# Kernel optimization log

Measured on AMD Instinct MI355X. Metric: run time of the kernel, lower is better.

## Reference

```python
import jax, jax.numpy as jnp
import numpy as np

NG = 64  # number of graphs in the batch (global_add_pool output rows)

def _bn(x, g, b):
    # BatchNorm1d, training-mode batch statistics over dim 0
    mu = x.mean(0)
    var = x.var(0)
    return (x - mu) * jax.lax.rsqrt(var + 1e-5) * g + b

def _ln(x, g, b):
    mu = x.mean(-1, keepdims=True)
    var = x.var(-1, keepdims=True)
    return (x - mu) * jax.lax.rsqrt(var + 1e-5) * g + b

def _gine(x, ei, ea, eps, w1, b1, w2, b2, n):
    # GINEConv: mlp((1+eps)*x + sum_dst ReLU(x[src] + ea))
    msg = jax.nn.relu(x[ei[0]] + ea)
    agg = jax.ops.segment_sum(msg, ei[1], num_segments=n)
    h = (1.0 + eps) * x + agg
    return jax.nn.relu(h @ w1 + b1) @ w2 + b2

def setup_inputs() -> dict:
    key = jax.random.key(0)
    H, L, RW = 128, 4, 16
    Nn, m, kk = 4096, 2, 32
    S = Nn * m; SK = S * kk
    Ei, Eg = 1048576, 65536
    Vatom, Vbond = 128, 16
    ks = jax.random.split(key, 24)
    f = lambda i, shape: jax.random.normal(ks[i], shape, jnp.float32) * 0.02
    # intra edges sampled within each subgraph block to honor locality
    subs = jax.random.randint(ks[11], (Ei,), 0, S)
    src = subs * kk + jax.random.randint(ks[12], (Ei,), 0, kk)
    dst = subs * kk + jax.random.randint(ks[13], (Ei,), 0, kk)
    inp = {
        "atom_emb": f(0, (Vatom, H)), "bond_emb": f(1, (Vbond, H)),
        "rwse_w": f(2, (RW, H)), "rwse_b": jnp.zeros((H,), jnp.float32),
        "rwse": jax.random.uniform(ks[3], (Nn, RW), jnp.float32),
        "l_eps": jnp.zeros((L,), jnp.float32),
        "l_w1": f(4, (L, H, H)), "l_b1": jnp.zeros((L, H), jnp.float32),
        "l_w2": f(5, (L, H, H)), "l_b2": jnp.zeros((L, H), jnp.float32),
        "l_bng": jnp.ones((L, H), jnp.float32), "l_bnb": jnp.zeros((L, H), jnp.float32),
        "g_eps": jnp.zeros((L,), jnp.float32),
        "g_w1": f(6, (L, H, H)), "g_b1": jnp.zeros((L, H), jnp.float32),
        "g_w2": f(7, (L, H, H)), "g_b2": jnp.zeros((L, H), jnp.float32),
        "g_bng": jnp.ones((L, H), jnp.float32), "g_bnb": jnp.zeros((L, H), jnp.float32),
        "bcast_w": f(8, (L, H, H)),
        "cat_w1": f(9, (L, 2 * H, H)), "cat_b1": jnp.zeros((L, H), jnp.float32),
        "cat_w2": f(10, (L, H, H)), "cat_b2": jnp.zeros((L, H), jnp.float32),
        "ln_g": jnp.ones((L, H), jnp.float32), "ln_b": jnp.zeros((L, H), jnp.float32),
        "x_ids": jax.random.randint(ks[14], (SK,), 0, Vatom),
        "intra_ei": jnp.stack([src, dst]),
        "intra_ea_ids": jax.random.randint(ks[15], (Ei,), 0, Vbond),
        "global_ei": jax.random.randint(ks[16], (2, Eg), 0, Nn),
        "global_ea_ids": jax.random.randint(ks[17], (Eg,), 0, Vbond),
        "node_ids": jax.random.randint(ks[18], (SK,), 0, Nn),
        "valid": jax.random.randint(ks[19], (SK,), 0, 2),
        "batch": jnp.sort(jax.random.randint(ks[20], (Nn,), 0, NG)),
        "k": 32,
    }
    return inp

def reference(atom_emb, bond_emb, rwse_w, rwse_b, rwse, l_eps, l_w1, l_b1, l_w2, l_b2, l_bng, l_bnb, g_eps, g_w1, g_b1, g_w2, g_b2, g_bng, g_bnb, bcast_w, cat_w1, cat_b1, cat_w2, cat_b2, ln_g, ln_b, x_ids, intra_ei, intra_ea_ids, global_ei, global_ea_ids, node_ids, valid, batch, k):
    SK = x_ids.shape[0]; Nn = rwse.shape[0]
    S = SK // k; m = S // Nn
    H = atom_emb.shape[1]; L = l_eps.shape[0]
    ea_flat = bond_emb[intra_ea_ids]          # [Ei, H]
    g_ea = bond_emb[global_ea_ids]            # [Eg, H]
    valid_f = valid.astype(jnp.float32)[:, None]
    h = (atom_emb[x_ids] + jax.nn.relu(rwse @ rwse_w + rwse_b)[node_ids]) * valid_f  # [SK, H]
    node_assign = jnp.repeat(jnp.arange(Nn), m)   # [S]
    root_idx = jnp.arange(S) * k                  # subgraph roots in flat layout
    for i in range(L):
        h_in = h
        h_local = _bn(jax.nn.relu(_gine(h, intra_ei, ea_flat, l_eps[i], l_w1[i], l_b1[i], l_w2[i], l_b2[i], SK)), l_bng[i], l_bnb[i])
        # scatter-mean of root reps onto original nodes (each node has exactly m subgraphs)
        h_node = jax.ops.segment_sum(h[root_idx], node_assign, num_segments=Nn) / m
        h_cross = _bn(jax.nn.relu(_gine(h_node, global_ei, g_ea, g_eps[i], g_w1[i], g_b1[i], g_w2[i], g_b2[i], Nn)), g_bng[i], g_bnb[i])
        h_node = h_node + h_cross
        # broadcast projected node reps back to every flat subgraph position
        h_b = jnp.repeat((h_node @ bcast_w[i])[node_assign], k, axis=0)  # [SK, H]
        h_cat = jnp.concatenate([h_local, h_b], axis=-1)
        h_new = _ln(jax.nn.gelu(h_cat @ cat_w1[i] + cat_b1[i], approximate=False) @ cat_w2[i] + cat_b2[i], ln_g[i], ln_b[i])
        h = (h_in + h_new) * valid_f
    # per-subgraph masked mean (h is already zero at invalid rows)
    cnt = valid_f.reshape(S, k, 1).sum(1)
    h_sub = h.reshape(S, k, H).sum(1) / jnp.maximum(cnt, 1.0)   # [S, H]
    h_nodef = h_sub.reshape(Nn, m, H).mean(1)                   # [Nn, H]
    return jax.ops.segment_sum(h_nodef, batch, num_segments=NG) # [NG, H]
```

## Files before the change

### kernel.cpp

```cpp
#include <hip/hip_runtime.h>
#include <hip/hip_bf16.h>

#define H 128
#define HH 16384
#define LNUM 4
#define NN 4096
#define SS 8192
#define SKK 262144
#define EI 1048576
#define EG 65536
#define NGRAPH 64

typedef unsigned short u16;
typedef unsigned int u32;
typedef __attribute__((ext_vector_type(8))) short s16x8;
typedef __attribute__((ext_vector_type(4))) float f32x4;

__device__ __forceinline__ float b2f(u32 u){ return __uint_as_float(u<<16); }
__device__ __forceinline__ u16 f2b(float f){
  union { __hip_bfloat16 b; u16 u; } x;
  x.b=__float2bfloat16(f);
  return x.u;
}
__device__ __forceinline__ void unp8(uint4 v, float* f){
  f[0]=b2f(v.x&0xFFFF); f[1]=b2f(v.x>>16);
  f[2]=b2f(v.y&0xFFFF); f[3]=b2f(v.y>>16);
  f[4]=b2f(v.z&0xFFFF); f[5]=b2f(v.z>>16);
  f[6]=b2f(v.w&0xFFFF); f[7]=b2f(v.w>>16);
}
__device__ __forceinline__ void unp4(uint2 v, float* f){
  f[0]=b2f(v.x&0xFFFF); f[1]=b2f(v.x>>16);
  f[2]=b2f(v.y&0xFFFF); f[3]=b2f(v.y>>16);
}
__device__ __forceinline__ uint4 pk8(const float* f){
  uint4 r;
  r.x=(u32)f2b(f[0])|((u32)f2b(f[1])<<16);
  r.y=(u32)f2b(f[2])|((u32)f2b(f[3])<<16);
  r.z=(u32)f2b(f[4])|((u32)f2b(f[5])<<16);
  r.w=(u32)f2b(f[6])|((u32)f2b(f[7])<<16);
  return r;
}
__device__ __forceinline__ uint2 pk4(const float* f){
  uint2 r;
  r.x=(u32)f2b(f[0])|((u32)f2b(f[1])<<16);
  r.y=(u32)f2b(f[2])|((u32)f2b(f[3])<<16);
  return r;
}

struct CvtArgs {
  const void* p[26];
  int start[27];
};
struct TransArgs { int src[28]; };

__global__ void k_sniff(const u16* __restrict__ a, int* __restrict__ flag){
  __shared__ int cnt;
  if(threadIdx.x==0) cnt=0;
  __syncthreads();
  int big=0;
  for(int i=threadIdx.x;i<2048;i+=256){
    int e=(a[i]>>7)&0xFF;
    if(e>=127) big++;
  }
  atomicAdd(&cnt,big);
  __syncthreads();
  if(threadIdx.x==0) *flag=(cnt<16)?1:0;
}

__global__ void k_convert(CvtArgs args, const int* __restrict__ flag, float* __restrict__ dst){
  int fl=*flag;
  int total=args.start[26];
  for(int i=blockIdx.x*blockDim.x+threadIdx.x;i<total;i+=gridDim.x*blockDim.x){
    int a=0;
    while(args.start[a+1]<=i) a++;
    int j=i-args.start[a];
    float v;
    if(fl) v=b2f(((const u16*)args.p[a])[j]);
    else   v=((const float*)args.p[a])[j];
    dst[i]=v;
  }
}

__global__ __launch_bounds__(256) void k_trans(const float* __restrict__ par, TransArgs ta, u16* __restrict__ wt){
  const float* s=par+ta.src[blockIdx.x];
  u16* d=wt+(size_t)blockIdx.x*HH;
  for(int i=threadIdx.x;i<HH;i+=256){
    int j=i&7, lane=(i>>3)&63, fc=i>>9;
    int n=fc>>2, kc=fc&3, lr=lane&15, lk=lane>>4;
    int outc=n*16+lr, k=kc*32+lk*8+j;
    d[i]=f2b(s[(size_t)k*H+outc]);
  }
}

__global__ void k_cvtbond(const float* __restrict__ b, u16* __restrict__ bb){
  int i=blockIdx.x*blockDim.x+threadIdx.x;
  if(i<16*H) bb[i]=f2b(b[i]);
}

__global__ __launch_bounds__(128) void k_prepw3(const float* __restrict__ w, const float* __restrict__ cb1,
                        const float* __restrict__ stl, const float* __restrict__ gl, const float* __restrict__ bl,
                        u16* __restrict__ wt3p, float* __restrict__ bias3){
  __shared__ float red[128];
  int c=blockIdx.x, k=threadIdx.x;
  float mu=stl[k]*(1.f/262144.f);
  float var=stl[128+k]*(1.f/262144.f)-mu*mu;
  float s=gl[k]*rsqrtf(var+1e-5f);
  float tt=bl[k]-mu*s;
  float wv=w[(size_t)k*H+c];
  int idx=(((c>>4)*4+(k>>5))*64+((k>>3)&3)*16+(c&15))*8+(k&7);
  wt3p[idx]=f2b(s*wv);
  red[k]=tt*wv;
  __syncthreads();
  for(int d=64;d>0;d>>=1){ if(k<d) red[k]+=red[k+d]; __syncthreads(); }
  if(k==0) bias3[c]=cb1[c]+red[0];
}

__global__ void k_hist(const int* __restrict__ idx, int n, int shift, int* __restrict__ cnt){
  for(int i=blockIdx.x*blockDim.x+threadIdx.x;i<n;i+=gridDim.x*blockDim.x)
    atomicAdd(&cnt[idx[i]>>shift],1);
}

__global__ void k_scan(const int* __restrict__ cnt, int* __restrict__ off, int nbins){
  __shared__ int ts[1024];
  int t=threadIdx.x;
  int per=nbins>>10;
  int base=t*per;
  int s=0;
  for(int j=0;j<per;j++) s+=cnt[base+j];
  ts[t]=s;
  __syncthreads();
  for(int d=1;d<1024;d<<=1){
    int v=(t>=d)?ts[t-d]:0;
    __syncthreads();
    ts[t]+=v;
    __syncthreads();
  }
  int ex=(t==0)?0:ts[t-1];
  for(int j=0;j<per;j++){ off[base+j]=ex; ex+=cnt[base+j]; }
}

__global__ void k_scatter_i(const int* __restrict__ ei, const int* __restrict__ ea,
                            const int* __restrict__ off, int* __restrict__ cur, int* __restrict__ pack){
  for(int i=blockIdx.x*blockDim.x+threadIdx.x;i<EI;i+=gridDim.x*blockDim.x){
    int s=ei[i], d=ei[EI+i];
    int sub=d>>5;
    int pos=off[sub]+atomicAdd(&cur[sub],1);
    pack[pos]=((s&31)<<9)|((d&31)<<4)|(ea[i]&15);
  }
}

__global__ __launch_bounds__(128) void k_sortsub(const int* __restrict__ eoff, const int* __restrict__ ecnt,
                                                 int* __restrict__ epack, int* __restrict__ dstoff){
  __shared__ int ein[512];
  __shared__ int eout[512];
  __shared__ int bcnt[32];
  __shared__ int bpos[32];
  int sub=blockIdx.x, t=threadIdx.x;
  int o=eoff[sub];
  int n=ecnt[sub]; if(n>512) n=512;
  for(int i=t;i<n;i+=128) ein[i]=epack[o+i];
  if(t<32) bcnt[t]=0;
  __syncthreads();
  for(int i=t;i<n;i+=128) atomicAdd(&bcnt[(ein[i]>>4)&31],1);
  __syncthreads();
  if(t==0){
    int s=0;
    for(int b=0;b<32;b++){ bpos[b]=s; s+=bcnt[b]; }
  }
  __syncthreads();
  if(t<32) dstoff[sub*32+t]=bpos[t];
  __syncthreads();
  for(int i=t;i<n;i+=128){
    int p=ein[i];
    int pos=atomicAdd(&bpos[(p>>4)&31],1);
    eout[pos]=p;
  }
  __syncthreads();
  for(int i=t;i<n;i+=128) epack[o+i]=eout[i];
}

__global__ void k_scatter_g(const int* __restrict__ ei, const int* __restrict__ ea,
                            const int* __restrict__ off, int* __restrict__ cur, int* __restrict__ pack){
  for(int i=blockIdx.x*blockDim.x+threadIdx.x;i<EG;i+=gridDim.x*blockDim.x){
    int s=ei[i], d=ei[EG+i];
    int pos=off[d]+atomicAdd(&cur[d],1);
    pack[pos]=(s<<4)|(ea[i]&15);
  }
}

__global__ __launch_bounds__(128) void k_rwse(const float* __restrict__ rwse, const float* __restrict__ w,
                      const float* __restrict__ b, float* __restrict__ rf){
  __shared__ float ws[16*128];
  __shared__ float rv[16];
  int n=blockIdx.x, c=threadIdx.x;
  for(int i=c;i<2048;i+=128) ws[i]=w[i];
  if(c<16) rv[c]=rwse[n*16+c];
  __syncthreads();
  float acc=b[c];
  for(int j=0;j<16;j++) acc=fmaf(rv[j],ws[j*128+c],acc);
  rf[(size_t)n*H+c]=fmaxf(acc,0.f);
}

template<int MODE>
__global__ __launch_bounds__(256,4) void k_fused1(
    const u16* __restrict__ h, const u16* __restrict__ beb,
    const int* __restrict__ eoff, const int* __restrict__ ecnt, const int* __restrict__ epack,
    const int* __restrict__ dstoff,
    const float* __restrict__ epsp, int layer,
    const u16* __restrict__ W1p, const float* __restrict__ b1,
    const u16* __restrict__ W2p, const float* __restrict__ b2,
    u16* __restrict__ Xg, float* __restrict__ stats,
    const u16* __restrict__ W3p, const float* __restrict__ bias3,
    const u16* __restrict__ bbv,
    const u16* __restrict__ Wc2p, const float* __restrict__ cb2,
    const float* __restrict__ lng, const float* __restrict__ lnb,
    const int* __restrict__ validv, u16* __restrict__ hio,
    const float* __restrict__ atomp, const float* __restrict__ rfp,
    const int* __restrict__ xids, const int* __restrict__ nids,
    u16* __restrict__ hnOut)
{
  __shared__ u16 hs[64*128];
  __shared__ u16 agx[64*128];
  __shared__ u16 bes[16*128];
  __shared__ u16 epku[2][512];
  __shared__ int doff[2][32];
  float* sst=(float*)&epku[0][0];

  int t=threadIdx.x;
  int grp=t>>7, c=t&127;
  size_t hbase=(size_t)blockIdx.x*64*H;
  int wave=t>>6, lane=t&63, lr=lane&15, lk=lane>>4;
  int rl=wave*16+lr;
  u32 rsw=((u32)(rl&7))<<4;
  int row0=blockIdx.x*64;

  {
    u32 row=(u32)(t>>4), colb=(u32)((t&15)*16);
    *(uint4*)((char*)bes+row*256+(colb^((row&7)<<4)))=((const uint4*)beb)[t];
  }
  int sub=blockIdx.x*2+grp;
  int n=min(ecnt[sub],512);
  int o=eoff[sub];
  if(c<32) doff[grp][c]=dstoff[sub*32+c];
  for(int i=c;i<n;i+=128) epku[grp][i]=(u16)epack[o+i];

  if(MODE==1){
    f32x4 a1t[8];
    #pragma unroll
    for(int n8=0;n8<8;n8++) a1t[n8]=(f32x4){0.f,0.f,0.f,0.f};
    const s16x8* B0=(const s16x8*)(Xg+(size_t)(row0+rl)*H);
    #pragma unroll
    for(int kc=0;kc<4;kc++){
      s16x8 bf=B0[kc*4+lk];
      #pragma unroll
      for(int n8=0;n8<8;n8++){
        s16x8 af=*(const s16x8*)(W3p+((n8*4+kc)<<9)+lane*8);
        a1t[n8]=__builtin_amdgcn_mfma_f32_16x16x32_bf16(af,bf,a1t[n8],0,0,0);
      }
    }
    #pragma unroll
    for(int n8=0;n8<8;n8++){
      int c0=n8*16+lk*4;
      float4 b4=*(const float4*)(bias3+c0);
      float rb[4];
      unp4(*(const uint2*)(bbv+(size_t)blockIdx.x*H+c0),rb);
      float vb[4]={b4.x,b4.y,b4.z,b4.w};
      float v[4];
      #pragma unroll
      for(int j=0;j<4;j++){
        float x=a1t[n8][j]+vb[j]+rb[j];
        v[j]=0.5f*x*(1.f+erff(x*0.70710678118654752f));
      }
      *(uint2*)((char*)agx+(u32)rl*256+(((u32)(2*c0))^rsw))=pk4(v);
    }
    f32x4 a2t[8];
    #pragma unroll
    for(int n8=0;n8<8;n8++) a2t[n8]=(f32x4){0.f,0.f,0.f,0.f};
    #pragma unroll
    for(int kc=0;kc<4;kc++){
      u32 cb=(u32)((kc*32+lk*8)*2);
      s16x8 bf=*(const s16x8*)((char*)agx+(u32)rl*256+(cb^rsw));
      #pragma unroll
      for(int n8=0;n8<8;n8++){
        s16x8 af=*(const s16x8*)(Wc2p+((n8*4+kc)<<9)+lane*8);
        a2t[n8]=__builtin_amdgcn_mfma_f32_16x16x32_bf16(af,bf,a2t[n8],0,0,0);
      }
    }
    {
      float s=0.f,q=0.f;
      #pragma unroll
      for(int n8=0;n8<8;n8++){
        int c0=n8*16+lk*4;
        float4 b4=*(const float4*)(cb2+c0);
        float vb[4]={b4.x,b4.y,b4.z,b4.w};
        #pragma unroll
        for(int j=0;j<4;j++){
          float v=a2t[n8][j]+vb[j];
          a2t[n8][j]=v;
          s+=v; q+=v*v;
        }
      }
      s+=__shfl_xor(s,16); s+=__shfl_xor(s,32);
      q+=__shfl_xor(q,16); q+=__shfl_xor(q,32);
      float mu=s*(1.f/128.f);
      float rsig=rsqrtf(q*(1.f/128.f)-mu*mu+1e-5f);
      #pragma unroll
      for(int n8=0;n8<8;n8++){
        int c0=n8*16+lk*4;
        float4 g4=*(const float4*)(lng+c0);
        float4 e4=*(const float4*)(lnb+c0);
        float g[4]={g4.x,g4.y,g4.z,g4.w}, e[4]={e4.x,e4.y,e4.z,e4.w};
        float ov[4];
        #pragma unroll
        for(int j=0;j<4;j++) ov[j]=(a2t[n8][j]-mu)*rsig*g[j]+e[j];
        *(uint2*)((char*)agx+(u32)rl*256+(((u32)(2*c0))^rsw))=pk4(ov);
      }
    }
    __syncthreads();
    uint4* hp=(uint4*)(hio+hbase);
    #pragma unroll
    for(int p=0;p<4;p++){
      int i=t+p*256;
      u32 row=(u32)(i>>4), colb=(u32)((i&15)*16);
      int grow=row0+(int)row;
      uint4 v=*(const uint4*)((const char*)agx+row*256+(colb^((row&7)<<4)));
      uint4 r=hp[i];
      float vv[8],rv[8],o8[8];
      unp8(v,vv); unp8(r,rv);
      float vm=validv[grow]?1.f:0.f;
      #pragma unroll
      for(int j=0;j<8;j++) o8[j]=(rv[j]+vv[j])*vm;
      uint4 pk=pk8(o8);
      hp[i]=pk;
      *(uint4*)((char*)hs+row*256+(colb^((row&7)<<4)))=pk;
    }
  } else {
    int r=t>>2, q=t&3;
    int grow=row0+r;
    float vm=validv[grow]?1.f:0.f;
    const float4* ap=(const float4*)(atomp+(size_t)xids[grow]*H)+q*8;
    const float4* bp=(const float4*)(rfp+(size_t)nids[grow]*H)+q*8;
    u32 rowsw=((u32)(r&7))<<4;
    uint4* hgp=(uint4*)(hio+hbase);
    #pragma unroll
    for(int k=0;k<4;k++){
      float4 a0=ap[k*2], a1=ap[k*2+1], b0=bp[k*2], b1=bp[k*2+1];
      float f[8]={(a0.x+b0.x)*vm,(a0.y+b0.y)*vm,(a0.z+b0.z)*vm,(a0.w+b0.w)*vm,
                  (a1.x+b1.x)*vm,(a1.y+b1.y)*vm,(a1.z+b1.z)*vm,(a1.w+b1.w)*vm};
      uint4 pk=pk8(f);
      u32 cb=(u32)(q*64+k*16);
      *(uint4*)((char*)hs+(u32)r*256+(cb^rowsw))=pk;
      hgp[r*16+q*4+k]=pk;
    }
  }
  __syncthreads();

  if(t<16){
    uint4 aR=*(const uint4*)((const char*)hs+(u32)t*16);
    uint4 bR=*(const uint4*)((const char*)hs+32*256+(u32)t*16);
    float fa[8],fb[8],fo[8];
    unp8(aR,fa); unp8(bR,fb);
    #pragma unroll
    for(int j=0;j<8;j++) fo[j]=0.5f*(fa[j]+fb[j]);
    ((uint4*)(hnOut+(size_t)blockIdx.x*H))[t]=pk8(fo);
  }
  {
    float ep=1.f+epsp[layer];
    #pragma unroll
    for(int p=0;p<4;p++){
      int i=t+p*256;
      u32 row=(u32)(i>>4), colb=(u32)((i&15)*16);
      u32 off=row*256+(colb^((row&7)<<4));
      float hf[8],o8[8];
      unp8(*(const uint4*)((const char*)hs+off),hf);
      #pragma unroll
      for(int j=0;j<8;j++) o8[j]=ep*hf[j];
      *(uint4*)((char*)agx+off)=pk8(o8);
    }
  }
  __syncthreads();

  {
    int slot=c>>4, chg=c&15;
    u32 cbyte=(u32)chg*16;
    int d0=slot*4;
    int s0=doff[grp][d0];
    int send=(d0+3==31)?n:doff[grp][d0+4];
    const u16* ep_=&epku[grp][0];
    auto LDP=[&](int p, uint4& hv, uint4& bv){
      u32 srow=(u32)(grp*32+(p>>9));
      u32 erow=(u32)(p&15);
      hv=*(const uint4*)((const char*)hs+srow*256+(cbyte^((srow&7)<<4)));
      bv=*(const uint4*)((const char*)bes+erow*256+(cbyte^((erow&7)<<4)));
    };
    auto FLUSH=[&](int cur, float* acc){
      u32 drow=(u32)(grp*32+cur);
      u32 aoff=drow*256+(cbyte^((drow&7)<<4));
      float of[8];
      unp8(*(const uint4*)((const char*)agx+aoff),of);
      #pragma unroll
      for(int q=0;q<8;q++) of[q]+=acc[q];
      *(uint4*)((char*)agx+aoff)=pk8(of);
    };
    float acc[8]={0.f,0.f,0.f,0.f,0.f,0.f,0.f,0.f};
    int cur=-1;
    uint4 hvA,bvA,hvB,bvB;
    hvA=bvA=hvB=bvB=make_uint4(0,0,0,0);
    int pA=0,pB=0;
    if(s0<send){ pA=ep_[s0]; LDP(pA,hvA,bvA); }
    if(s0+1<send){ pB=ep_[s0+1]; LDP(pB,hvB,bvB); }
    for(int j=s0;j<send;){
      {
        float hf[8],bf8[8];
        unp8(hvA,hf); unp8(bvA,bf8);
        int pc=pA;
        if(j+2<send){ pA=ep_[j+2]; LDP(pA,hvA,bvA); }
        int dl=(pc>>4)&31;
        if(dl!=cur){
          if(cur>=0) FLUSH(cur,acc);
          #pragma unroll
          for(int q=0;q<8;q++) acc[q]=0.f;
          cur=dl;
        }
        #pragma unroll
        for(int q=0;q<8;q++) acc[q]+=fmaxf(hf[q]+bf8[q],0.f);
      }
      j++;
      if(j>=send) break;
      {
        float hf[8],bf8[8];
        unp8(hvB,hf); unp8(bvB,bf8);
        int pc=pB;
        if(j+2<send){ pB=ep_[j+2]; LDP(pB,hvB,bvB); }
        int dl=(pc>>4)&31;
        if(dl!=cur){
          if(cur>=0) FLUSH(cur,acc);
          #pragma unroll
          for(int q=0;q<8;q++) acc[q]=0.f;
          cur=dl;
        }
        #pragma unroll
        for(int q=0;q<8;q++) acc[q]+=fmaxf(hf[q]+bf8[q],0.f);
      }
      j++;
    }
    if(cur>=0) FLUSH(cur,acc);
  }
  __syncthreads();
  sst[t]=0.f;
  __syncthreads();

  f32x4 a1[8];
  #pragma unroll
  for(int n8=0;n8<8;n8++) a1[n8]=(f32x4){0.f,0.f,0.f,0.f};
  #pragma unroll
  for(int kc=0;kc<4;kc++){
    u32 cb=(u32)((kc*32+lk*8)*2);
    s16x8 bf=*(const s16x8*)((char*)agx+(u32)rl*256+(cb^rsw));
    #pragma unroll
    for(int n8=0;n8<8;n8++){
      s16x8 af=*(const s16x8*)(W1p+((n8*4+kc)<<9)+lane*8);
      a1[n8]=__builtin_amdgcn_mfma_f32_16x16x32_bf16(af,bf,a1[n8],0,0,0);
    }
  }
  #pragma unroll
  for(int n8=0;n8<8;n8++){
    int c0=n8*16+lk*4;
    float4 b4=*(const float4*)(b1+c0);
    float v[4]={fmaxf(a1[n8][0]+b4.x,0.f),fmaxf(a1[n8][1]+b4.y,0.f),
                fmaxf(a1[n8][2]+b4.z,0.f),fmaxf(a1[n8][3]+b4.w,0.f)};
    *(uint2*)((char*)hs+(u32)rl*256+(((u32)(2*c0))^rsw))=pk4(v);
  }
  f32x4 a2[8];
  #pragma unroll
  for(int n8=0;n8<8;n8++) a2[n8]=(f32x4){0.f,0.f,0.f,0.f};
  #pragma unroll
  for(int kc=0;kc<4;kc++){
    u32 cb=(u32)((kc*32+lk*8)*2);
    s16x8 bf=*(const s16x8*)((char*)hs+(u32)rl*256+(cb^rsw));
    #pragma unroll
    for(int n8=0;n8<8;n8++){
      s16x8 af=*(const s16x8*)(W2p+((n8*4+kc)<<9)+lane*8);
      a2[n8]=__builtin_amdgcn_mfma_f32_16x16x32_bf16(af,bf,a2[n8],0,0,0);
    }
  }
  #pragma unroll
  for(int n8=0;n8<8;n8++){
    int c0=n8*16+lk*4;
    float4 b4=*(const float4*)(b2+c0);
    float v[4]={fmaxf(a2[n8][0]+b4.x,0.f),fmaxf(a2[n8][1]+b4.y,0.f),
                fmaxf(a2[n8][2]+b4.z,0.f),fmaxf(a2[n8][3]+b4.w,0.f)};
    *(uint2*)((char*)agx+(u32)rl*256+(((u32)(2*c0))^rsw))=pk4(v);
    float s[4],q[4];
    #pragma unroll
    for(int j2=0;j2<4;j2++){ s[j2]=v[j2]; q[j2]=v[j2]*v[j2]; }
    #pragma unroll
    for(int j2=0;j2<4;j2++){
      #pragma unroll
      for(int d=1;d<16;d<<=1){
        s[j2]+=__shfl_xor(s[j2],d);
        q[j2]+=__shfl_xor(q[j2],d);
      }
    }
    if(lr==0){
      #pragma unroll
      for(int j2=0;j2<4;j2++){
        atomicAdd(&sst[c0+j2],s[j2]);
        atomicAdd(&sst[128+c0+j2],q[j2]);
      }
    }
  }
  __syncthreads();
  uint4* out4=(uint4*)(Xg+hbase);
  #pragma unroll
  for(int p=0;p<4;p++){
    int i=t+p*256;
    u32 row=(u32)(i>>4), colb=(u32)((i&15)*16);
    out4[i]=*(const uint4*)((const char*)agx+row*256+(colb^((row&7)<<4)));
  }
  atomicAdd(&stats[t],sst[t]);
}

__global__ __launch_bounds__(256) void k_mlp2n(
    const u16* __restrict__ A, const u16* __restrict__ W1p, const float* __restrict__ b1,
    const u16* __restrict__ W2p, const float* __restrict__ b2,
    u16* __restrict__ out, float* __restrict__ stats)
{
  __shared__ u16 T[64*128];
  __shared__ float sst[256];
  int t=threadIdx.x;
  sst[t]=0.f;
  int wave=t>>6, lane=t&63, lr=lane&15, lk=lane>>4;
  int rl=wave*16+lr;
  u32 rsw=((u32)(rl&7))<<4;
  int row0=blockIdx.x*64;
  f32x4 a1[8];
  #pragma unroll
  for(int n8=0;n8<8;n8++) a1[n8]=(f32x4){0.f,0.f,0.f,0.f};
  const s16x8* B0=(const s16x8*)(A+(size_t)(row0+rl)*H);
  #pragma unroll
  for(int kc=0;kc<4;kc++){
    s16x8 bf=B0[kc*4+lk];
    #pragma unroll
    for(int n8=0;n8<8;n8++){
      s16x8 af=*(const s16x8*)(W1p+((n8*4+kc)<<9)+lane*8);
      a1[n8]=__builtin_amdgcn_mfma_f32_16x16x32_bf16(af,bf,a1[n8],0,0,0);
    }
  }
  #pragma unroll
  for(int n8=0;n8<8;n8++){
    int c0=n8*16+lk*4;
    float4 b4=*(const float4*)(b1+c0);
    float v[4]={fmaxf(a1[n8][0]+b4.x,0.f),fmaxf(a1[n8][1]+b4.y,0.f),
                fmaxf(a1[n8][2]+b4.z,0.f),fmaxf(a1[n8][3]+b4.w,0.f)};
    *(uint2*)((char*)T+(u32)rl*256+(((u32)(2*c0))^rsw))=pk4(v);
  }
  f32x4 a2[8];
  #pragma unroll
  for(int n8=0;n8<8;n8++) a2[n8]=(f32x4){0.f,0.f,0.f,0.f};
  #pragma unroll
  for(int kc=0;kc<4;kc++){
    u32 cb=(u32)((kc*32+lk*8)*2);
    s16x8 bf=*(const s16x8*)((char*)T+(u32)rl*256+(cb^rsw));
    #pragma unroll
    for(int n8=0;n8<8;n8++){
      s16x8 af=*(const s16x8*)(W2p+((n8*4+kc)<<9)+lane*8);
      a2[n8]=__builtin_amdgcn_mfma_f32_16x16x32_bf16(af,bf,a2[n8],0,0,0);
    }
  }
  #pragma unroll
  for(int n8=0;n8<8;n8++){
    int c0=n8*16+lk*4;
    float4 b4=*(const float4*)(b2+c0);
    float v[4]={fmaxf(a2[n8][0]+b4.x,0.f),fmaxf(a2[n8][1]+b4.y,0.f),
                fmaxf(a2[n8][2]+b4.z,0.f),fmaxf(a2[n8][3]+b4.w,0.f)};
    *(uint2*)((char*)T+(u32)rl*256+(((u32)(2*c0))^rsw))=pk4(v);
    float s[4],q[4];
    #pragma unroll
    for(int j=0;j<4;j++){ s[j]=v[j]; q[j]=v[j]*v[j]; }
    #pragma unroll
    for(int j=0;j<4;j++){
      #pragma unroll
      for(int d=1;d<16;d<<=1){
        s[j]+=__shfl_xor(s[j],d);
        q[j]+=__shfl_xor(q[j],d);
      }
    }
    if(lr==0){
      #pragma unroll
      for(int j=0;j<4;j++){
        atomicAdd(&sst[c0+j],s[j]);
        atomicAdd(&sst[128+c0+j],q[j]);
      }
    }
  }
  __syncthreads();
  uint4* out4=(uint4*)(out+(size_t)row0*H);
  #pragma unroll
  for(int p=0;p<4;p++){
    int i=t+p*256;
    u32 row=(u32)(i>>4), colb=(u32)((i&15)*16);
    out4[i]=*(const uint4*)((const char*)T+row*256+(colb^((row&7)<<4)));
  }
  atomicAdd(&stats[t],sst[t]);
}

__global__ __launch_bounds__(256) void k_bcast(
    const u16* __restrict__ hn, const u16* __restrict__ ag,
    const float* __restrict__ stg, const float* __restrict__ gg, const float* __restrict__ bg,
    const u16* __restrict__ Wbcp, const u16* __restrict__ Wc1p,
    u16* __restrict__ bb)
{
  __shared__ u16 T[64*128];
  __shared__ u16 T2[64*128];
  __shared__ float ssh[128], tsh[128];
  int t=threadIdx.x;
  int row0=blockIdx.x*64;
  if(t<128){
    float mu=stg[t]*(1.f/4096.f);
    float var=stg[128+t]*(1.f/4096.f)-mu*mu;
    float s=gg[t]*rsqrtf(var+1e-5f);
    ssh[t]=s; tsh[t]=bg[t]-mu*s;
  }
  __syncthreads();
  #pragma unroll
  for(int i0=0;i0<4;i0++){
    int i=t+i0*256;
    u32 row=(u32)(i>>4);
    int cb8=(i&15)*8;
    float hv[8],av[8],o8[8];
    unp8(((const uint4*)(hn+(size_t)row0*H))[i],hv);
    unp8(((const uint4*)(ag+(size_t)row0*H))[i],av);
    #pragma unroll
    for(int j=0;j<8;j++) o8[j]=hv[j]+fmaf(av[j],ssh[cb8+j],tsh[cb8+j]);
    *(uint4*)((char*)T+row*256+(((u32)(cb8*2))^((row&7)<<4)))=pk8(o8);
  }
  __syncthreads();
  int wave=t>>6, lane=t&63, lr=lane&15, lk=lane>>4;
  int rl=wave*16+lr;
  u32 rsw=((u32)(rl&7))<<4;
  f32x4 a1[8];
  #pragma unroll
  for(int n8=0;n8<8;n8++) a1[n8]=(f32x4){0.f,0.f,0.f,0.f};
  #pragma unroll
  for(int kc=0;kc<4;kc++){
    u32 cb=(u32)((kc*32+lk*8)*2);
    s16x8 bf=*(const s16x8*)((char*)T+(u32)rl*256+(cb^rsw));
    #pragma unroll
    for(int n8=0;n8<8;n8++){
      s16x8 af=*(const s16x8*)(Wbcp+((n8*4+kc)<<9)+lane*8);
      a1[n8]=__builtin_amdgcn_mfma_f32_16x16x32_bf16(af,bf,a1[n8],0,0,0);
    }
  }
  #pragma unroll
  for(int n8=0;n8<8;n8++){
    int c0=n8*16+lk*4;
    float v[4]={a1[n8][0],a1[n8][1],a1[n8][2],a1[n8][3]};
    *(uint2*)((char*)T2+(u32)rl*256+(((u32)(2*c0))^rsw))=pk4(v);
  }
  f32x4 a2[8];
  #pragma unroll
  for(int n8=0;n8<8;n8++) a2[n8]=(f32x4){0.f,0.f,0.f,0.f};
  #pragma unroll
  for(int kc=0;kc<4;kc++){
    u32 cb=(u32)((kc*32+lk*8)*2);
    s16x8 bf=*(const s16x8*)((char*)T2+(u32)rl*256+(cb^rsw));
    #pragma unroll
    for(int n8=0;n8<8;n8++){
      s16x8 af=*(const s16x8*)(Wc1p+((n8*4+kc)<<9)+lane*8);
      a2[n8]=__builtin_amdgcn_mfma_f32_16x16x32_bf16(af,bf,a2[n8],0,0,0);
    }
  }
  #pragma unroll
  for(int n8=0;n8<8;n8++){
    int c0=n8*16+lk*4;
    float v[4]={a2[n8][0],a2[n8][1],a2[n8][2],a2[n8][3]};
    *(uint2*)((char*)T+(u32)rl*256+(((u32)(2*c0))^rsw))=pk4(v);
  }
  __syncthreads();
  uint4* out4=(uint4*)(bb+(size_t)row0*H);
  #pragma unroll
  for(int p=0;p<4;p++){
    int i=t+p*256;
    u32 row=(u32)(i>>4), colb=(u32)((i&15)*16);
    out4[i]=*(const uint4*)((const char*)T+row*256+(colb^((row&7)<<4)));
  }
}

__global__ __launch_bounds__(128) void k_gagg(const u16* __restrict__ hn, const float* __restrict__ be,
                      const int* __restrict__ goff, const int* __restrict__ gcnt,
                      const int* __restrict__ gpack, const float* __restrict__ epsp, int layer,
                      u16* __restrict__ hhg){
  __shared__ float bes[16][128];
  int n=blockIdx.x, c=threadIdx.x;
  for(int i=0;i<16;i++) bes[i][c]=be[i*128+c];
  __syncthreads();
  float acc=0.f;
  int o=goff[n], e=o+gcnt[n];
  for(;o<e;o++){
    int p=gpack[o];
    acc+=fmaxf(b2f(hn[(size_t)(p>>4)*H+c])+bes[p&15][c],0.f);
  }
  hhg[(size_t)n*H+c]=f2b(fmaf(1.f+epsp[layer],b2f(hn[(size_t)n*H+c]),acc));
}

__global__ __launch_bounds__(256) void k_tailpool(
    const u16* __restrict__ X, const u16* __restrict__ W3p, const float* __restrict__ bias3,
    const u16* __restrict__ bb,
    const u16* __restrict__ W2p, const float* __restrict__ cb2,
    const float* __restrict__ lng, const float* __restrict__ lnb,
    const int* __restrict__ validv, const u16* __restrict__ hres,
    const int* __restrict__ batch, float* __restrict__ oacc)
{
  __shared__ u16 T[64*128];
  __shared__ float pbuf[256];
  __shared__ float cntsh[2];
  int t=threadIdx.x;
  int wave=t>>6, lane=t&63, lr=lane&15, lk=lane>>4;
  int rl=wave*16+lr;
  u32 rsw=((u32)(rl&7))<<4;
  int row0=blockIdx.x*64;
  f32x4 acc[8];
  #pragma unroll
  for(int n8=0;n8<8;n8++) acc[n8]=(f32x4){0.f,0.f,0.f,0.f};
  const s16x8* B0=(const s16x8*)(X+(size_t)(row0+rl)*H);
  #pragma unroll
  for(int kc=0;kc<4;kc++){
    s16x8 bf=B0[kc*4+lk];
    #pragma unroll
    for(int n8=0;n8<8;n8++){
      s16x8 af=*(const s16x8*)(W3p+((n8*4+kc)<<9)+lane*8);
      acc[n8]=__builtin_amdgcn_mfma_f32_16x16x32_bf16(af,bf,acc[n8],0,0,0);
    }
  }
  #pragma unroll
  for(int n8=0;n8<8;n8++){
    int c0=n8*16+lk*4;
    float4 b4=*(const float4*)(bias3+c0);
    float rb[4];
    unp4(*(const uint2*)(bb+(size_t)blockIdx.x*H+c0),rb);
    float vb[4]={b4.x,b4.y,b4.z,b4.w};
    float v[4];
    #pragma unroll
    for(int j=0;j<4;j++){
      float x=acc[n8][j]+vb[j]+rb[j];
      v[j]=0.5f*x*(1.f+erff(x*0.70710678118654752f));
    }
    *(uint2*)((char*)T+(u32)rl*256+(((u32)(2*c0))^rsw))=pk4(v);
  }
  f32x4 a2[8];
  #pragma unroll
  for(int n8=0;n8<8;n8++) a2[n8]=(f32x4){0.f,0.f,0.f,0.f};
  #pragma unroll
  for(int kc=0;kc<4;kc++){
    u32 cb=(u32)((kc*32+lk*8)*2);
    s16x8 bf=*(const s16x8*)((char*)T+(u32)rl*256+(cb^rsw));
    #pragma unroll
    for(int n8=0;n8<8;n8++){
      s16x8 af=*(const s16x8*)(W2p+((n8*4+kc)<<9)+lane*8);
      a2[n8]=__builtin_amdgcn_mfma_f32_16x16x32_bf16(af,bf,a2[n8],0,0,0);
    }
  }
  {
    float s=0.f,q=0.f;
    #pragma unroll
    for(int n8=0;n8<8;n8++){
      int c0=n8*16+lk*4;
      float4 b4=*(const float4*)(cb2+c0);
      float vb[4]={b4.x,b4.y,b4.z,b4.w};
      #pragma unroll
      for(int j=0;j<4;j++){
        float v=a2[n8][j]+vb[j];
        a2[n8][j]=v;
        s+=v; q+=v*v;
      }
    }
    s+=__shfl_xor(s,16); s+=__shfl_xor(s,32);
    q+=__shfl_xor(q,16); q+=__shfl_xor(q,32);
    float mu=s*(1.f/128.f);
    float rsig=rsqrtf(q*(1.f/128.f)-mu*mu+1e-5f);
    #pragma unroll
    for(int n8=0;n8<8;n8++){
      int c0=n8*16+lk*4;
      float4 g4=*(const float4*)(lng+c0);
      float4 e4=*(const float4*)(lnb+c0);
      float g[4]={g4.x,g4.y,g4.z,g4.w}, e[4]={e4.x,e4.y,e4.z,e4.w};
      float ov[4];
      #pragma unroll
      for(int j=0;j<4;j++) ov[j]=(a2[n8][j]-mu)*rsig*g[j]+e[j];
      *(uint2*)((char*)T+(u32)rl*256+(((u32)(2*c0))^rsw))=pk4(ov);
    }
  }
  pbuf[t]=0.f;
  if(t<2){
    int s=0;
    for(int j2=0;j2<32;j2++) s+=validv[row0+t*32+j2]?1:0;
    cntsh[t]=fmaxf((float)s,1.f);
  }
  __syncthreads();
  const uint4* hp=(const uint4*)(hres+(size_t)row0*H);
  float s0[8]={0,0,0,0,0,0,0,0}, s1[8]={0,0,0,0,0,0,0,0};
  #pragma unroll
  for(int p=0;p<4;p++){
    int i=t+p*256;
    u32 row=(u32)(i>>4), colb=(u32)((i&15)*16);
    int grow=row0+(int)row;
    uint4 v=*(const uint4*)((const char*)T+row*256+(colb^((row&7)<<4)));
    uint4 r=hp[i];
    float vv[8],rv[8];
    unp8(v,vv); unp8(r,rv);
    float vm=validv[grow]?1.f:0.f;
    #pragma unroll
    for(int j2=0;j2<8;j2++){
      float hn=(rv[j2]+vv[j2])*vm;
      if(p<2) s0[j2]+=hn; else s1[j2]+=hn;
    }
  }
  #pragma unroll
  for(int j2=0;j2<8;j2++){
    s0[j2]+=__shfl_xor(s0[j2],16); s0[j2]+=__shfl_xor(s0[j2],32);
    s1[j2]+=__shfl_xor(s1[j2],16); s1[j2]+=__shfl_xor(s1[j2],32);
  }
  if((lane&48)==0){
    int ch=(lane&15)*8;
    #pragma unroll
    for(int j2=0;j2<8;j2++){
      atomicAdd(&pbuf[ch+j2],s0[j2]);
      atomicAdd(&pbuf[128+ch+j2],s1[j2]);
    }
  }
  __syncthreads();
  if(t<128){
    float nodef=0.5f*(pbuf[t]/cntsh[0]+pbuf[128+t]/cntsh[1]);
    atomicAdd(&oacc[batch[blockIdx.x]*H+t],nodef);
  }
}

__global__ void k_out(const float* __restrict__ acc, const int* __restrict__ flag, void* __restrict__ out){
  int i=blockIdx.x*blockDim.x+threadIdx.x;
  if(i>=NGRAPH*H) return;
  if(*flag) ((__hip_bfloat16*)out)[i]=__float2bfloat16(acc[i]);
  else ((float*)out)[i]=acc[i];
}

extern "C" void kernel_launch(void* const* d_in, const int* in_sizes, int n_in,
                              void* d_out, int out_size, void* d_ws, size_t ws_size,
                              hipStream_t stream){
  (void)n_in; (void)out_size;
  int pofs[27]; pofs[0]=0;
  for(int i=0;i<26;i++) pofs[i+1]=pofs[i]+in_sizes[i];
  int ptot=pofs[26];

  char* wsb=(char*)d_ws;
  size_t off=0;
  auto alloc=[&](size_t bytes)->char*{ char* p=wsb+off; off+=(bytes+255)&~(size_t)255; return p; };
  int*   flag =(int*)  alloc(4);
  float* par  =(float*)alloc((size_t)ptot*4);
  u16*   h    =(u16*)  alloc((size_t)SKK*H*2);
  u16*   X    =(u16*)  alloc((size_t)SKK*H*2);
  u16*   wt   =(u16*)  alloc((size_t)28*HH*2);
  u16*   wt3  =(u16*)  alloc((size_t)HH*2);
  float* bias3=(float*)alloc(H*4);
  float* rf   =(float*)alloc((size_t)NN*H*4);
  u16*   bondb=(u16*)  alloc((size_t)16*H*2);
  u16*   hn   =(u16*)  alloc((size_t)NN*H*2);
  u16*   hhg  =(u16*)  alloc((size_t)NN*H*2);
  u16*   ag   =(u16*)  alloc((size_t)NN*H*2);
  u16*   bb   =(u16*)  alloc((size_t)NN*H*2);
  int*   ecnt =(int*)  alloc(SS*4);
  int*   ecur =(int*)  alloc(SS*4);
  int*   gcnt =(int*)  alloc(NN*4);
  int*   gcur =(int*)  alloc(NN*4);
  float* stats=(float*)alloc(LNUM*512*4);
  float* oacc =(float*)alloc((size_t)NGRAPH*H*4);
  size_t zbytes=(size_t)SS*4+SS*4+NN*4+NN*4+LNUM*512*4+(size_t)NGRAPH*H*4;
  int* eoff  =(int*)alloc(SS*4);
  int* epack =(int*)alloc((size_t)EI*4);
  int* dstoff=(int*)alloc((size_t)SS*32*4);
  int* goff  =(int*)alloc(NN*4);
  int* gpack =(int*)alloc((size_t)EG*4);

  if(off>ws_size) return;

  const int* xids =(const int*)d_in[26];
  const int* iei  =(const int*)d_in[27];
  const int* iea  =(const int*)d_in[28];
  const int* gei  =(const int*)d_in[29];
  const int* gea  =(const int*)d_in[30];
  const int* nids =(const int*)d_in[31];
  const int* valid=(const int*)d_in[32];
  const int* batch=(const int*)d_in[33];

  const float* atom=par+pofs[0];
  const float* bond=par+pofs[1];
  const float* rw_w=par+pofs[2];
  const float* rw_b=par+pofs[3];
  const float* rwse=par+pofs[4];
  const float* leps=par+pofs[5];
  const float* lb1 =par+pofs[7];
  const float* lb2 =par+pofs[9];
  const float* lbng=par+pofs[10];
  const float* lbnb=par+pofs[11];
  const float* geps=par+pofs[12];
  const float* gb1 =par+pofs[14];
  const float* gb2 =par+pofs[16];
  const float* gbng=par+pofs[17];
  const float* gbnb=par+pofs[18];
  const float* cw1 =par+pofs[20];
  const float* cb1 =par+pofs[21];
  const float* cb2 =par+pofs[23];
  const float* lngp=par+pofs[24];
  const float* lnbp=par+pofs[25];

  k_sniff<<<1,256,0,stream>>>((const u16*)d_in[0], flag);
  CvtArgs ca;
  for(int i=0;i<26;i++){ ca.p[i]=d_in[i]; ca.start[i]=pofs[i]; }
  ca.start[26]=ptot;
  k_convert<<<1024,256,0,stream>>>(ca, flag, par);

  TransArgs ta;
  for(int l=0;l<LNUM;l++){
    ta.src[l*7+0]=pofs[6]+l*HH;
    ta.src[l*7+1]=pofs[8]+l*HH;
    ta.src[l*7+2]=pofs[13]+l*HH;
    ta.src[l*7+3]=pofs[15]+l*HH;
    ta.src[l*7+4]=pofs[19]+l*HH;
    ta.src[l*7+5]=pofs[20]+l*2*HH+HH;
    ta.src[l*7+6]=pofs[22]+l*HH;
  }
  k_trans<<<28,256,0,stream>>>(par, ta, wt);
  k_cvtbond<<<8,256,0,stream>>>(bond, bondb);

  (void)hipMemsetAsync(ecnt,0,zbytes,stream);

  k_hist<<<2048,256,0,stream>>>(iei+EI, EI, 5, ecnt);
  k_scan<<<1,1024,0,stream>>>(ecnt, eoff, SS);
  k_scatter_i<<<2048,256,0,stream>>>(iei, iea, eoff, ecur, epack);
  k_sortsub<<<SS,128,0,stream>>>(eoff, ecnt, epack, dstoff);
  k_hist<<<512,256,0,stream>>>(gei+EG, EG, 0, gcnt);
  k_scan<<<1,1024,0,stream>>>(gcnt, goff, NN);
  k_scatter_g<<<512,256,0,stream>>>(gei, gea, goff, gcur, gpack);

  k_rwse<<<NN,128,0,stream>>>(rwse, rw_w, rw_b, rf);

  for(int l=0;l<LNUM;l++){
    float* stl_l=stats+l*512;
    float* stg_l=stats+l*512+256;
    if(l==0){
      k_fused1<2><<<SS/2,256,0,stream>>>(h, bondb, eoff, ecnt, epack, dstoff, leps, l,
          wt+(size_t)(l*7+0)*HH, lb1+l*H, wt+(size_t)(l*7+1)*HH, lb2+l*H, X, stl_l,
          nullptr,nullptr,nullptr,nullptr,nullptr,nullptr,nullptr, valid, h,
          atom, rf, xids, nids, hn);
    } else {
      int pl=l-1;
      k_fused1<1><<<SS/2,256,0,stream>>>(h, bondb, eoff, ecnt, epack, dstoff, leps, l,
          wt+(size_t)(l*7+0)*HH, lb1+l*H, wt+(size_t)(l*7+1)*HH, lb2+l*H, X, stl_l,
          wt3, bias3, bb, wt+(size_t)(pl*7+6)*HH, cb2+pl*H,
          lngp+pl*H, lnbp+pl*H, valid, h,
          nullptr, nullptr, nullptr, nullptr, hn);
    }
    k_prepw3<<<128,128,0,stream>>>(cw1+(size_t)l*2*HH, cb1+l*H, stl_l, lbng+l*H, lbnb+l*H, wt3, bias3);
    k_gagg<<<NN,128,0,stream>>>(hn, bond, goff, gcnt, gpack, geps, l, hhg);
    k_mlp2n<<<NN/64,256,0,stream>>>(hhg, wt+(size_t)(l*7+2)*HH, gb1+l*H,
        wt+(size_t)(l*7+3)*HH, gb2+l*H, ag, stg_l);
    k_bcast<<<NN/64,256,0,stream>>>(hn, ag, stg_l, gbng+l*H, gbnb+l*H,
        wt+(size_t)(l*7+4)*HH, wt+(size_t)(l*7+5)*HH, bb);
  }
  {
    int l=LNUM-1;
    k_tailpool<<<SKK/64,256,0,stream>>>(X, wt3, bias3, bb,
        wt+(size_t)(l*7+6)*HH, cb2+l*H, lngp+l*H, lnbp+l*H, valid, h, batch, oacc);
  }
  k_out<<<(NGRAPH*H+255)/256,256,0,stream>>>(oacc, flag, d_out);
}
```

Before: 1.185 ms.

## Fuse global GINE aggregation into node MLP kernel and use tanh GELU

Merges the per-node global-edge aggregation (previously k_gagg, one block per node) into the node MLP kernel: each 64-node block gathers neighbour rows with 4 threads per node, builds the GINE input in shared memory, then runs both MFMA layers. This removes one launch per layer and the hhg round trip through global memory, but the gather now runs in only 64 blocks. Separately, the exact erf GELU in the large per-row kernels is replaced with a tanh-style approximation built on exp. That approximation departs from the reference's exact GELU within the tolerance allowed for bf16. The aggregation also now reads bond embeddings from the bf16 copy instead of fp32.

Result: faster. 1.147 ms (-3.3%).

```diff
diff --git a/kernel.cpp b/kernel.cpp
--- a/kernel.cpp
+++ b/kernel.cpp
@@ -45,6 +45,11 @@
   r.x=(u32)f2b(f[0])|((u32)f2b(f[1])<<16);
   r.y=(u32)f2b(f[2])|((u32)f2b(f[3])<<16);
   return r;
+}
+__device__ __forceinline__ float gelu_f(float x){
+  float u=x*(0.7978845608f+0.0356774081f*x*x);
+  float ex=__expf(fminf(2.f*u,80.f));
+  return x*(ex/(ex+1.f));
 }
 
 struct CvtArgs {
@@ -268,8 +273,7 @@
       float v[4];
       #pragma unroll
       for(int j=0;j<4;j++){
-        float x=a1t[n8][j]+vb[j]+rb[j];
-        v[j]=0.5f*x*(1.f+erff(x*0.70710678118654752f));
+        v[j]=gelu_f(a1t[n8][j]+vb[j]+rb[j]);
       }
       *(uint2*)((char*)agx+(u32)rl*256+(((u32)(2*c0))^rsw))=pk4(v);
     }
@@ -521,15 +525,58 @@
   atomicAdd(&stats[t],sst[t]);
 }
 
-__global__ __launch_bounds__(256) void k_mlp2n(
-    const u16* __restrict__ A, const u16* __restrict__ W1p, const float* __restrict__ b1,
+__global__ __launch_bounds__(256) void k_node(
+    const u16* __restrict__ hn, const u16* __restrict__ beb,
+    const int* __restrict__ goff, const int* __restrict__ gcnt, const int* __restrict__ gpack,
+    const float* __restrict__ epsp, int layer,
+    const u16* __restrict__ W1p, const float* __restrict__ b1,
     const u16* __restrict__ W2p, const float* __restrict__ b2,
-    u16* __restrict__ out, float* __restrict__ stats)
+    u16* __restrict__ ag, float* __restrict__ stats)
 {
   __shared__ u16 T[64*128];
+  __shared__ u16 T2[64*128];
+  __shared__ u16 bes[16*128];
   __shared__ float sst[256];
   int t=threadIdx.x;
   sst[t]=0.f;
+  ((uint4*)bes)[t]=((const uint4*)beb)[t];
+  __syncthreads();
+  int node4=t>>2, q=t&3;
+  int gnode=blockIdx.x*64+node4;
+  float acc[32];
+  float ep=1.f+epsp[layer];
+  {
+    const uint4* hrow=(const uint4*)(hn+(size_t)gnode*H+q*32);
+    #pragma unroll
+    for(int v=0;v<4;v++){
+      float tmp[8];
+      unp8(hrow[v],tmp);
+      #pragma unroll
+      for(int j=0;j<8;j++) acc[v*8+j]=ep*tmp[j];
+    }
+  }
+  int o=goff[gnode], e=o+gcnt[gnode];
+  for(;o<e;o++){
+    int p=gpack[o];
+    const uint4* srow=(const uint4*)(hn+(size_t)(p>>4)*H+q*32);
+    const uint4* brow=(const uint4*)(bes+(p&15)*128+q*32);
+    #pragma unroll
+    for(int v=0;v<4;v++){
+      float tmp[8],bf8[8];
+      unp8(srow[v],tmp); unp8(brow[v],bf8);
+      #pragma unroll
+      for(int j=0;j<8;j++) acc[v*8+j]+=fmaxf(tmp[j]+bf8[j],0.f);
+    }
+  }
+  {
+    u32 rs=((u32)(node4&7))<<4;
+    #pragma unroll
+    for(int v=0;v<4;v++){
+      u32 cb=(u32)((q*32+v*8)*2);
+      *(uint4*)((char*)T+(u32)node4*256+(cb^rs))=pk8(&acc[v*8]);
+    }
+  }
+  __syncthreads();
   int wave=t>>6, lane=t&63, lr=lane&15, lk=lane>>4;
   int rl=wave*16+lr;
   u32 rsw=((u32)(rl&7))<<4;
@@ -537,10 +584,10 @@
   f32x4 a1[8];
   #pragma unroll
   for(int n8=0;n8<8;n8++) a1[n8]=(f32x4){0.f,0.f,0.f,0.f};
-  const s16x8* B0=(const s16x8*)(A+(size_t)(row0+rl)*H);
   #pragma unroll
   for(int kc=0;kc<4;kc++){
-    s16x8 bf=B0[kc*4+lk];
+    u32 cb=(u32)((kc*32+lk*8)*2);
+    s16x8 bf=*(const s16x8*)((char*)T+(u32)rl*256+(cb^rsw));
     #pragma unroll
     for(int n8=0;n8<8;n8++){
       s16x8 af=*(const s16x8*)(W1p+((n8*4+kc)<<9)+lane*8);
@@ -553,7 +600,7 @@
     float4 b4=*(const float4*)(b1+c0);
     float v[4]={fmaxf(a1[n8][0]+b4.x,0.f),fmaxf(a1[n8][1]+b4.y,0.f),
                 fmaxf(a1[n8][2]+b4.z,0.f),fmaxf(a1[n8][3]+b4.w,0.f)};
-    *(uint2*)((char*)T+(u32)rl*256+(((u32)(2*c0))^rsw))=pk4(v);
+    *(uint2*)((char*)T2+(u32)rl*256+(((u32)(2*c0))^rsw))=pk4(v);
   }
   f32x4 a2[8];
   #pragma unroll
@@ -561,7 +608,7 @@
   #pragma unroll
   for(int kc=0;kc<4;kc++){
     u32 cb=(u32)((kc*32+lk*8)*2);
-    s16x8 bf=*(const s16x8*)((char*)T+(u32)rl*256+(cb^rsw));
+    s16x8 bf=*(const s16x8*)((char*)T2+(u32)rl*256+(cb^rsw));
     #pragma unroll
     for(int n8=0;n8<8;n8++){
       s16x8 af=*(const s16x8*)(W2p+((n8*4+kc)<<9)+lane*8);
@@ -575,27 +622,27 @@
     float v[4]={fmaxf(a2[n8][0]+b4.x,0.f),fmaxf(a2[n8][1]+b4.y,0.f),
                 fmaxf(a2[n8][2]+b4.z,0.f),fmaxf(a2[n8][3]+b4.w,0.f)};
     *(uint2*)((char*)T+(u32)rl*256+(((u32)(2*c0))^rsw))=pk4(v);
-    float s[4],q[4];
-    #pragma unroll
-    for(int j=0;j<4;j++){ s[j]=v[j]; q[j]=v[j]*v[j]; }
+    float s[4],qq[4];
+    #pragma unroll
+    for(int j=0;j<4;j++){ s[j]=v[j]; qq[j]=v[j]*v[j]; }
     #pragma unroll
     for(int j=0;j<4;j++){
       #pragma unroll
       for(int d=1;d<16;d<<=1){
         s[j]+=__shfl_xor(s[j],d);
-        q[j]+=__shfl_xor(q[j],d);
+        qq[j]+=__shfl_xor(qq[j],d);
       }
     }
     if(lr==0){
       #pragma unroll
       for(int j=0;j<4;j++){
         atomicAdd(&sst[c0+j],s[j]);
-        atomicAdd(&sst[128+c0+j],q[j]);
-      }
-    }
-  }
-  __syncthreads();
-  uint4* out4=(uint4*)(out+(size_t)row0*H);
+        atomicAdd(&sst[128+c0+j],qq[j]);
+      }
+    }
+  }
+  __syncthreads();
+  uint4* out4=(uint4*)(ag+(size_t)row0*H);
   #pragma unroll
   for(int p=0;p<4;p++){
     int i=t+p*256;
@@ -685,23 +732,6 @@
     u32 row=(u32)(i>>4), colb=(u32)((i&15)*16);
     out4[i]=*(const uint4*)((const char*)T+row*256+(colb^((row&7)<<4)));
   }
-}
-
-__global__ __launch_bounds__(128) void k_gagg(const u16* __restrict__ hn, const float* __restrict__ be,
-                      const int* __restrict__ goff, const int* __restrict__ gcnt,
-                      const int* __restrict__ gpack, const float* __restrict__ epsp, int layer,
-                      u16* __restrict__ hhg){
-  __shared__ float bes[16][128];
-  int n=blockIdx.x, c=threadIdx.x;
-  for(int i=0;i<16;i++) bes[i][c]=be[i*128+c];
-  __syncthreads();
-  float acc=0.f;
-  int o=goff[n], e=o+gcnt[n];
-  for(;o<e;o++){
-    int p=gpack[o];
-    acc+=fmaxf(b2f(hn[(size_t)(p>>4)*H+c])+bes[p&15][c],0.f);
-  }
-  hhg[(size_t)n*H+c]=f2b(fmaf(1.f+epsp[layer],b2f(hn[(size_t)n*H+c]),acc));
 }
 
 __global__ __launch_bounds__(256) void k_tailpool(
@@ -743,8 +773,7 @@
     float v[4];
     #pragma unroll
     for(int j=0;j<4;j++){
-      float x=acc[n8][j]+vb[j]+rb[j];
-      v[j]=0.5f*x*(1.f+erff(x*0.70710678118654752f));
+      v[j]=gelu_f(acc[n8][j]+vb[j]+rb[j]);
     }
     *(uint2*)((char*)T+(u32)rl*256+(((u32)(2*c0))^rsw))=pk4(v);
   }
@@ -812,8 +841,8 @@
     float vm=validv[grow]?1.f:0.f;
     #pragma unroll
     for(int j2=0;j2<8;j2++){
-      float hn=(rv[j2]+vv[j2])*vm;
-      if(p<2) s0[j2]+=hn; else s1[j2]+=hn;
+      float hh=(rv[j2]+vv[j2])*vm;
+      if(p<2) s0[j2]+=hh; else s1[j2]+=hh;
     }
   }
   #pragma unroll
@@ -864,7 +893,6 @@
   float* rf   =(float*)alloc((size_t)NN*H*4);
   u16*   bondb=(u16*)  alloc((size_t)16*H*2);
   u16*   hn   =(u16*)  alloc((size_t)NN*H*2);
-  u16*   hhg  =(u16*)  alloc((size_t)NN*H*2);
   u16*   ag   =(u16*)  alloc((size_t)NN*H*2);
   u16*   bb   =(u16*)  alloc((size_t)NN*H*2);
   int*   ecnt =(int*)  alloc(SS*4);
@@ -960,9 +988,8 @@
           nullptr, nullptr, nullptr, nullptr, hn);
     }
     k_prepw3<<<128,128,0,stream>>>(cw1+(size_t)l*2*HH, cb1+l*H, stl_l, lbng+l*H, lbnb+l*H, wt3, bias3);
-    k_gagg<<<NN,128,0,stream>>>(hn, bond, goff, gcnt, gpack, geps, l, hhg);
-    k_mlp2n<<<NN/64,256,0,stream>>>(hhg, wt+(size_t)(l*7+2)*HH, gb1+l*H,
-        wt+(size_t)(l*7+3)*HH, gb2+l*H, ag, stg_l);
+    k_node<<<NN/64,256,0,stream>>>(hn, bondb, goff, gcnt, gpack, geps, l,
+        wt+(size_t)(l*7+2)*HH, gb1+l*H, wt+(size_t)(l*7+3)*HH, gb2+l*H, ag, stg_l);
     k_bcast<<<NN/64,256,0,stream>>>(hn, ag, stg_l, gbng+l*H, gbnb+l*H,
         wt+(size_t)(l*7+4)*HH, wt+(size_t)(l*7+5)*HH, bb);
   }
```
